# Kernel tuning notes

Measured on AMD Instinct MI355X. Metric: run time of the kernel, lower is better.

Reference implementation:

```python
import jax, jax.numpy as jnp
import numpy as np

N_NODES = 100000
N_EDGES = 1600000
NEG_SLOPE = 0.2
EPS = 1e-6


def setup_inputs() -> dict:
    key = jax.random.key(0)
    ks = jax.random.split(key, 14)
    s = 0.1  # weight init scale
    return {
        "x": jax.random.normal(ks[0], (N_NODES, 64), jnp.float32),
        "src": jax.random.randint(ks[1], (N_EDGES,), 0, N_NODES, jnp.int32),
        "dst": jax.random.randint(ks[2], (N_EDGES,), 0, N_NODES, jnp.int32),
        "W0": s * jax.random.normal(ks[3], (64, 128), jnp.float32),
        "al0": s * jax.random.normal(ks[4], (4, 32), jnp.float32),
        "ar0": s * jax.random.normal(ks[5], (4, 32), jnp.float32),
        "W1": s * jax.random.normal(ks[6], (128, 128), jnp.float32),
        "al1": s * jax.random.normal(ks[7], (4, 32), jnp.float32),
        "ar1": s * jax.random.normal(ks[8], (4, 32), jnp.float32),
        "resW1": s * jax.random.normal(ks[9], (128, 128), jnp.float32),
        "W2": s * jax.random.normal(ks[10], (128, 32), jnp.float32),
        "al2": s * jax.random.normal(ks[11], (1, 32), jnp.float32),
        "ar2": s * jax.random.normal(ks[12], (1, 32), jnp.float32),
        "resW2": s * jax.random.normal(ks[13], (128, 32), jnp.float32),
    }


def gat_conv(h, src, dst, W, al, ar, resW):
    """DGL-style GATConv. h: [N, Fin]; returns [N, H, D]."""
    H, D = al.shape
    feat = (h @ W).reshape(-1, H, D)                       # [N,H,D]
    el = jnp.sum(feat * al, axis=-1)                       # [N,H]
    er = jnp.sum(feat * ar, axis=-1)                       # [N,H]
    e = jax.nn.leaky_relu(el[src] + er[dst], NEG_SLOPE)    # [E,H]
    # segment softmax over destination nodes
    m = jax.ops.segment_max(e, dst, num_segments=N_NODES)  # [N,H]
    ex = jnp.exp(e - m[dst])                               # [E,H]
    denom = jax.ops.segment_sum(ex, dst, num_segments=N_NODES)
    alpha = ex / denom[dst]                                # [E,H]
    msg = alpha[:, :, None] * feat[src]                    # [E,H,D]
    rst = jax.ops.segment_sum(msg, dst, num_segments=N_NODES)  # [N,H,D]
    if resW is not None:
        rst = rst + (h @ resW).reshape(-1, H, D)
    return rst


def pairnorm_scs(x, scale=1.0):
    # 'PN-SCS' mode: scale-individually then center by original column mean
    col_mean = jnp.mean(x, axis=0)
    rownorm = jnp.sqrt(EPS + jnp.sum(x * x, axis=1, keepdims=True))
    return scale * x / rownorm - col_mean


def reference(x, src, dst, W0, al0, ar0, W1, al1, ar1, resW1, W2, al2, ar2, resW2):
    # layer 0: no residual, activation applied outside
    h = gat_conv(x, src, dst, W0, al0, ar0, None)          # [N,4,32]
    h = jax.nn.elu(h.reshape(h.shape[0], -1))              # [N,128]
    h = pairnorm_scs(h)
    # middle layer: residual + internal ELU (DGL applies activation inside),
    # then the outer loop flattens and applies ELU again
    h = jax.nn.elu(gat_conv(h, src, dst, W1, al1, ar1, resW1))  # [N,4,32]
    h = jax.nn.elu(h.reshape(h.shape[0], -1))              # [N,128]
    h = pairnorm_scs(h)
    # final layer: residual, mean over heads
    h = gat_conv(h, src, dst, W2, al2, ar2, resW2)         # [N,1,32]
    h = jnp.mean(h, axis=1)                                # [N,32]
    # dgl.mean_nodes readout on a single graph -> mean over nodes
    return jnp.mean(h, axis=0)                             # [32]
```

## Files before the change

kernel.cpp:

```cpp
#include <hip/hip_runtime.h>


typedef __attribute__((ext_vector_type(8))) short s8v;
typedef __attribute__((ext_vector_type(4))) float f4v;
typedef __attribute__((ext_vector_type(2))) float f2v;
typedef __attribute__((ext_vector_type(2))) _Float16 h2;
typedef __attribute__((ext_vector_type(4))) _Float16 h4;

__device__ __forceinline__ unsigned short f2bf(float f) {
  unsigned int x = __float_as_uint(f);
  x += 0x7fffu + ((x >> 16) & 1u);
  return (unsigned short)(x >> 16);
}
__device__ __forceinline__ float bf2f(unsigned short u) {
  return __uint_as_float(((unsigned int)u) << 16);
}
__device__ __forceinline__ unsigned short f2h(float f) {
  _Float16 h = (_Float16)f;
  return __builtin_bit_cast(unsigned short, h);
}
__device__ __forceinline__ unsigned char f2fp8(float v) {
  return (unsigned char)(__builtin_amdgcn_cvt_pk_fp8_f32(v, v, 0, false) & 0xff);
}
__device__ __forceinline__ float lrelu(float x) { return fmaxf(x, 0.2f * x); }
__device__ __forceinline__ float elu1(float x) { return x > 0.f ? x : __expf(x) - 1.f; }

__device__ __forceinline__ void pack_one(const float* W, const float* al, const float* ar,
                                         const float* resW, unsigned short* out,
                                         int K, int M, int BF, int H, int RES0, int t) {
  int c = t / K, k = t - c * K;
  float v = 0.f;
  if (c < BF) {
    v = W[k * BF + c];
  } else if (c < BF + H) {
    int h = c - BF;
    float s = 0.f;
    for (int d = 0; d < 32; d++) s += W[k * BF + h * 32 + d] * al[h * 32 + d];
    v = s;
  } else if (c < BF + 2 * H) {
    int h = c - BF - H;
    float s = 0.f;
    for (int d = 0; d < 32; d++) s += W[k * BF + h * 32 + d] * ar[h * 32 + d];
    v = s;
  } else if (c >= RES0) {
    v = resW[k * (M - RES0) + (c - RES0)];
  }
  unsigned short hi = f2bf(v);
  out[c * K + k] = hi;
  out[M * K + c * K + k] = f2bf(v - bf2f(hi));
}

__global__ __launch_bounds__(256) void hist_pack_k(const int* __restrict__ dst,
                                                   int* __restrict__ bhist, int E, int NB, int chunk, int P2B,
                                                   const float* __restrict__ W0, const float* __restrict__ al0,
                                                   const float* __restrict__ ar0,
                                                   const float* __restrict__ W1, const float* __restrict__ al1,
                                                   const float* __restrict__ ar1, const float* __restrict__ resW1,
                                                   const float* __restrict__ W2, const float* __restrict__ al2,
                                                   const float* __restrict__ ar2, const float* __restrict__ resW2,
                                                   unsigned short* __restrict__ w0t, unsigned short* __restrict__ w1t,
                                                   unsigned short* __restrict__ w2t) {
  if ((int)blockIdx.x < P2B) {
    __shared__ int h[512];
    for (int b = threadIdx.x; b < NB; b += 256) h[b] = 0;
    __syncthreads();
    int e0 = blockIdx.x * chunk;
    int e1 = min(E, e0 + chunk);
    for (int e = e0 + threadIdx.x; e < e1; e += 256) atomicAdd(&h[dst[e] >> 8], 1);
    __syncthreads();
    for (int b = threadIdx.x; b < NB; b += 256)
      bhist[(size_t)b * P2B + blockIdx.x] = h[b];
  } else {
    const int n0 = 144 * 64, n1 = 272 * 128, n2 = 80 * 128;
    int t = ((int)blockIdx.x - P2B) * 256 + threadIdx.x;
    if (t < n0) {
      pack_one(W0, al0, ar0, nullptr, w0t, 64, 144, 128, 4, 144, t);
    } else if (t < n0 + n1) {
      pack_one(W1, al1, ar1, resW1, w1t, 128, 272, 128, 4, 144, t - n0);
    } else if (t < n0 + n1 + n2) {
      pack_one(W2, al2, ar2, resW2, w2t, 128, 80, 32, 1, 48, t - n0 - n1);
    }
  }
}

__global__ __launch_bounds__(256) void pscan1(int* __restrict__ arr, int* __restrict__ bsum, int Nn) {
  __shared__ int s[256];
  int t = threadIdx.x;
  int base = blockIdx.x * 1024 + t * 4;
  int v0 = (base + 0 < Nn) ? arr[base + 0] : 0;
  int v1 = (base + 1 < Nn) ? arr[base + 1] : 0;
  int v2 = (base + 2 < Nn) ? arr[base + 2] : 0;
  int v3 = (base + 3 < Nn) ? arr[base + 3] : 0;
  s[t] = v0 + v1 + v2 + v3;
  __syncthreads();
  for (int off = 1; off < 256; off <<= 1) {
    int xv = (t >= off) ? s[t - off] : 0;
    __syncthreads();
    s[t] += xv;
    __syncthreads();
  }
  int excl = t ? s[t - 1] : 0;
  if (t == 255) bsum[blockIdx.x] = s[255];
  if (base + 0 < Nn) { arr[base + 0] = excl; excl += v0; }
  if (base + 1 < Nn) { arr[base + 1] = excl; excl += v1; }
  if (base + 2 < Nn) { arr[base + 2] = excl; excl += v2; }
  if (base + 3 < Nn) { arr[base + 3] = excl; }
}

__global__ __launch_bounds__(256) void pscan2(int* __restrict__ arr, const int* __restrict__ bsum,
                                              int Nn, int nb) {
  __shared__ int s[256];
  int t = threadIdx.x;
  s[t] = (t < nb) ? bsum[t] : 0;
  __syncthreads();
  for (int off = 1; off < 256; off <<= 1) {
    int xv = (t >= off) ? s[t - off] : 0;
    __syncthreads();
    s[t] += xv;
    __syncthreads();
  }
  int bb = blockIdx.x;
  int pref = bb ? s[bb - 1] : 0;
  if (pref != 0) {
    int base = bb * 1024 + t * 4;
    if (base + 0 < Nn) arr[base + 0] += pref;
    if (base + 1 < Nn) arr[base + 1] += pref;
    if (base + 2 < Nn) arr[base + 2] += pref;
    if (base + 3 < Nn) arr[base + 3] += pref;
  }
}

__global__ __launch_bounds__(256) void bscatter_k(const int* __restrict__ src, const int* __restrict__ dst,
                                                  const int* __restrict__ seg, unsigned int* __restrict__ ebuf,
                                                  int E, int NB, int chunk) {
  __shared__ int cur[512];
  for (int b = threadIdx.x; b < NB; b += 256)
    cur[b] = seg[(size_t)b * gridDim.x + blockIdx.x];
  __syncthreads();
  int e0 = blockIdx.x * chunk;
  int e1 = min(E, e0 + chunk);
  for (int e = e0 + threadIdx.x; e < e1; e += 256) {
    int d = dst[e];
    int pos = atomicAdd(&cur[d >> 8], 1);
    ebuf[pos] = ((unsigned int)src[e] << 8) | (unsigned int)(d & 255);
  }
}

__global__ __launch_bounds__(256) void fscatter_k(const unsigned int* __restrict__ ebuf,
                                                  const int* __restrict__ seg,
                                                  int* __restrict__ csr_src,
                                                  int* __restrict__ counts, int* __restrict__ rsp,
                                                  int E, int NB, int P2B, int Nn) {
  __shared__ int cnt[256];
  __shared__ int sc[256];
  __shared__ int cur[256];
  int b = blockIdx.x;
  int t = threadIdx.x;
  cnt[t] = 0;
  __syncthreads();
  int bstart = seg[(size_t)b * P2B];
  int bend = (b + 1 < NB) ? seg[(size_t)(b + 1) * P2B] : E;
  for (int e = bstart + t; e < bend; e += 256)
    atomicAdd(&cnt[ebuf[e] & 255u], 1);
  __syncthreads();
  int v = cnt[t];
  sc[t] = v;
  __syncthreads();
  for (int off = 1; off < 256; off <<= 1) {
    int xv = (t >= off) ? sc[t - off] : 0;
    __syncthreads();
    sc[t] += xv;
    __syncthreads();
  }
  int base = bstart + (t ? sc[t - 1] : 0);
  int node = (b << 8) + t;
  if (node < Nn) { counts[node] = v; rsp[node] = base; }
  cur[t] = base;
  __syncthreads();
  for (int e = bstart + t; e < bend; e += 256) {
    unsigned int sd = ebuf[e];
    int pos = atomicAdd(&cur[sd & 255u], 1);
    csr_src[pos] = (int)(sd >> 8);
  }
}

__global__ __launch_bounds__(256) void cmw_k(const float* __restrict__ colsum,
                                             const unsigned short* __restrict__ wt,
                                             float* __restrict__ cmw, int K, int M, float invN) {
  int c = blockIdx.x * 256 + threadIdx.x;
  if (c >= M) return;
  float s = 0.f;
  for (int k = 0; k < K; k++)
    s += colsum[k] * (bf2f(wt[c * K + k]) + bf2f(wt[(size_t)M * K + c * K + k]));
  cmw[c] = s * invN;
}

template <int K, int M, int R, int CG, int BF, int H, int RES0, bool AF32, bool CMW>
__global__ __launch_bounds__(256) void gemm_bf16(const void* __restrict__ Av,
                                                 const unsigned short* __restrict__ Bt,
                                                 const float* __restrict__ cmw,
                                                 unsigned char* __restrict__ feat8,
                                                 float* __restrict__ el, float* __restrict__ er,
                                                 unsigned short* __restrict__ resh, int nRowTiles) {
  int wv = (int)((blockIdx.x * blockDim.x + threadIdx.x) >> 6);
  int rowGroup = wv / CG;
  int cg = wv - rowGroup * CG;
  int tile0 = rowGroup * R;
  if (tile0 >= nRowTiles) return;
  int lane = threadIdx.x & 63;
  int r = lane & 15, q = lane >> 4;
  s8v afrag[R][K / 32];
#pragma unroll
  for (int rr = 0; rr < R; rr++) {
    if constexpr (AF32) {
      const float* arow = (const float*)Av + (size_t)((tile0 + rr) * 16 + r) * K + q * 8;
#pragma unroll
      for (int kk = 0; kk < K / 32; kk++) {
        s8v v;
#pragma unroll
        for (int j = 0; j < 8; j++) v[j] = (short)f2bf(arow[kk * 32 + j]);
        afrag[rr][kk] = v;
      }
    } else {
      const unsigned short* arow = (const unsigned short*)Av + (size_t)((tile0 + rr) * 16 + r) * K + q * 8;
#pragma unroll
      for (int kk = 0; kk < K / 32; kk++) afrag[rr][kk] = *(const s8v*)(arow + kk * 32);
    }
  }
  for (int ct = cg; ct < M / 16; ct += CG) {
    const unsigned short* brow = Bt + (size_t)(ct * 16 + r) * K + q * 8;
    s8v bhi[K / 32], blo[K / 32];
#pragma unroll
    for (int kk = 0; kk < K / 32; kk++) {
      bhi[kk] = *(const s8v*)(brow + kk * 32);
      blo[kk] = *(const s8v*)(brow + (size_t)M * K + kk * 32);
    }
    int col = ct * 16 + r;
    float cmwv = 0.f;
    if constexpr (CMW) cmwv = cmw[col];
#pragma unroll
    for (int rr = 0; rr < R; rr++) {
      f4v acc = {0.f, 0.f, 0.f, 0.f};
#pragma unroll
      for (int kk = 0; kk < K / 32; kk++) {
        acc = __builtin_amdgcn_mfma_f32_16x16x32_bf16(afrag[rr][kk], bhi[kk], acc, 0, 0, 0);
        acc = __builtin_amdgcn_mfma_f32_16x16x32_bf16(afrag[rr][kk], blo[kk], acc, 0, 0, 0);
      }
      int row0 = (tile0 + rr) * 16 + q * 4;
#pragma unroll
      for (int i = 0; i < 4; i++) {
        float v = acc[i] - cmwv;
        size_t row = (size_t)(row0 + i);
        if (col < BF) {
          feat8[row * BF + col] = f2fp8(v);
        } else if (col < BF + H) {
          el[row * H + (col - BF)] = v;
        } else if (col < BF + 2 * H) {
          er[row * H + (col - BF - H)] = v;
        } else if (RES0 < M && col >= RES0) {
          resh[row * (M - RES0) + (col - RES0)] = f2h(v);
        }
      }
    }
  }
}

template <int MODE>
__global__ __launch_bounds__(256) void aggregate4(const unsigned char* __restrict__ feat8,
                                                  const float* __restrict__ el4,
                                                  const float* __restrict__ er4,
                                                  const int* __restrict__ csr_src,
                                                  const int* __restrict__ rsp,
                                                  const int* __restrict__ counts,
                                                  const unsigned short* __restrict__ resh,
                                                  unsigned short* __restrict__ vbf,
                                                  float* __restrict__ rnrm, int Nn) {
  int n = (int)((blockIdx.x * blockDim.x + threadIdx.x) >> 6);
  if (n >= Nn) return;
  int lane = threadIdx.x & 63;
  int start = __builtin_amdgcn_readfirstlane(rsp[n]);
  int deg = __builtin_amdgcn_readfirstlane(counts[n]);
  int chunks = (deg + 15) >> 4;
  int slot = lane >> 2, h = lane & 3;
  float ern = er4[(size_t)n * 4 + h];
  int hl = lane >> 4;
  unsigned dby = (unsigned)lane << 1;
  f2v a01 = {0.f, 0.f};
  float dsum = 0.f;
  float elv = el4[(size_t)csr_src[start + slot] * 4 + h];
  for (int c = 0; c < chunks; c++) {
    const int* csp = csr_src + start + (c << 4);
    int sj[16];
#pragma unroll
    for (int j = 0; j < 16; j++) sj[j] = csp[j];
    float e = elv + ern;
    float exv = (((c << 4) + slot) < deg) ? __expf(fmaxf(e, 0.2f * e)) : 0.f;
    dsum += exv;
    if (c + 1 < chunks) elv = el4[(size_t)csp[16 + slot] * 4 + h];
#pragma unroll
    for (int j = 0; j < 16; j++) {
      float aw = __shfl(exv, (j << 2) | hl);
      unsigned short u = *(const unsigned short*)(feat8 + (((unsigned)sj[j] << 7) + dby));
      f2v fv = __builtin_amdgcn_cvt_pk_f32_fp8((int)u, false);
      f2v aw2 = {aw, aw};
      a01 = __builtin_elementwise_fma(fv, aw2, a01);
    }
  }
#pragma unroll
  for (int off = 4; off < 64; off <<= 1) dsum += __shfl_xor(dsum, off);
  float inv = dsum > 0.f ? 1.f / dsum : 0.f;
  float invh = __shfl(inv, hl);
  float v0, v1;
  if (MODE == 1) {
    h2 rr = *(const h2*)(resh + (size_t)n * 128 + lane * 2);
    v0 = elu1(elu1(a01[0] * invh + (float)rr[0]));
    v1 = elu1(elu1(a01[1] * invh + (float)rr[1]));
  } else {
    v0 = elu1(a01[0] * invh);
    v1 = elu1(a01[1] * invh);
  }
  float ss = v0 * v0 + v1 * v1;
#pragma unroll
  for (int off = 1; off < 64; off <<= 1) ss += __shfl_xor(ss, off);
  float rn = sqrtf(1e-6f + ss);
  float ri = 1.f / rn;
  unsigned int pk = (unsigned int)f2bf(v0 * ri) | ((unsigned int)f2bf(v1 * ri) << 16);
  *(unsigned int*)((char*)vbf + ((size_t)n << 8) + (lane << 2)) = pk;
  if (lane == 0) rnrm[n] = rn;
}

__global__ __launch_bounds__(256) void aggregate1(const unsigned char* __restrict__ feat8,
                                                  const float* __restrict__ el1,
                                                  const float* __restrict__ er1,
                                                  const int* __restrict__ csr_src,
                                                  const int* __restrict__ rsp,
                                                  const int* __restrict__ counts,
                                                  const unsigned short* __restrict__ res2h,
                                                  float* __restrict__ out2, int Nn) {
  int n = (int)((blockIdx.x * blockDim.x + threadIdx.x) >> 6);
  if (n >= Nn) return;
  int lane = threadIdx.x & 63;
  int start = __builtin_amdgcn_readfirstlane(rsp[n]);
  int deg = __builtin_amdgcn_readfirstlane(counts[n]);
  int chunks = (deg + 15) >> 4;
  int l16 = lane & 15;
  float ern = er1[n];
  int g = lane >> 3;
  unsigned dofs4 = (unsigned)(lane & 7) << 2;
  f2v acc01 = {0.f, 0.f}, acc23 = {0.f, 0.f};
  float dsum = 0.f;
  int sA = csr_src[start + l16];
  float elv = el1[sA];
  for (int c = 0; c < chunks; c++) {
    const int* csp = csr_src + start + (c << 4);
    float exv = (((c << 4) + l16) < deg) ? __expf(lrelu(elv + ern)) : 0.f;
    dsum += exv;
    int sAc = sA;
    if (c + 1 < chunks) {
      sA = csp[16 + l16];
      elv = el1[sA];
    }
#pragma unroll
    for (int t = 0; t < 2; t++) {
      int j = (t << 3) + g;
      int sj = __shfl(sAc, j);
      float aw = __shfl(exv, j);
      f2v aw2 = {aw, aw};
      unsigned int u = *(const unsigned int*)(feat8 + (((unsigned)sj << 5) + dofs4));
      f2v fa = __builtin_amdgcn_cvt_pk_f32_fp8((int)u, false);
      f2v fb = __builtin_amdgcn_cvt_pk_f32_fp8((int)u, true);
      acc01 = __builtin_elementwise_fma(fa, aw2, acc01);
      acc23 = __builtin_elementwise_fma(fb, aw2, acc23);
    }
  }
#pragma unroll
  for (int off = 1; off < 16; off <<= 1) dsum += __shfl_xor(dsum, off);
  float inv = dsum > 0.f ? 1.f / dsum : 0.f;
#pragma unroll
  for (int off = 8; off < 64; off <<= 1) {
    acc01[0] += __shfl_xor(acc01[0], off);
    acc01[1] += __shfl_xor(acc01[1], off);
    acc23[0] += __shfl_xor(acc23[0], off);
    acc23[1] += __shfl_xor(acc23[1], off);
  }
  if (lane < 8) {
    h4 rr = *(const h4*)(res2h + (size_t)n * 32 + (lane << 2));
    float4 o;
    o.x = acc01[0] * inv + (float)rr[0];
    o.y = acc01[1] * inv + (float)rr[1];
    o.z = acc23[0] * inv + (float)rr[2];
    o.w = acc23[1] * inv + (float)rr[3];
    *(float4*)(out2 + (size_t)n * 32 + (lane << 2)) = o;
  }
}

__global__ __launch_bounds__(256) void colsum_k(const unsigned short* __restrict__ vbf,
                                                const float* __restrict__ rnrm,
                                                float* __restrict__ colsum, int Nn) {
  __shared__ float ls[256];
  int tid = threadIdx.x;
  int c = tid & 127, rsub = tid >> 7;
  float cs = 0.f;
  for (int r = blockIdx.x * 2 + rsub; r < Nn; r += gridDim.x * 2)
    cs += bf2f(vbf[(size_t)r * 128 + c]) * rnrm[r];
  ls[tid] = cs;
  __syncthreads();
  if (tid < 128) atomicAdd(&colsum[tid], ls[tid] + ls[tid + 128]);
}

__global__ __launch_bounds__(256) void final_reduce(const float* __restrict__ out2,
                                                    float* __restrict__ outsum, int Nn) {
  __shared__ float ls[32];
  if (threadIdx.x < 32) ls[threadIdx.x] = 0.f;
  __syncthreads();
  int d = threadIdx.x & 31, rl = threadIdx.x >> 5;
  float acc = 0.f;
  for (int n = blockIdx.x * 8 + rl; n < Nn; n += gridDim.x * 8)
    acc += out2[(size_t)n * 32 + d];
  atomicAdd(&ls[d], acc);
  __syncthreads();
  if (threadIdx.x < 32) atomicAdd(&outsum[threadIdx.x], ls[threadIdx.x]);
}

__global__ void finalize_k(const float* __restrict__ outsum, float* __restrict__ out, float invN) {
  int t = threadIdx.x;
  if (t < 32) out[t] = outsum[t] * invN;
}

extern "C" void kernel_launch(void* const* d_in, const int* in_sizes, int n_in,
                              void* d_out, int out_size, void* d_ws, size_t ws_size,
                              hipStream_t stream) {
  const float* x     = (const float*)d_in[0];
  const int*   src   = (const int*)d_in[1];
  const int*   dst   = (const int*)d_in[2];
  const float* W0    = (const float*)d_in[3];
  const float* al0   = (const float*)d_in[4];
  const float* ar0   = (const float*)d_in[5];
  const float* W1    = (const float*)d_in[6];
  const float* al1   = (const float*)d_in[7];
  const float* ar1   = (const float*)d_in[8];
  const float* resW1 = (const float*)d_in[9];
  const float* W2    = (const float*)d_in[10];
  const float* al2   = (const float*)d_in[11];
  const float* ar2   = (const float*)d_in[12];
  const float* resW2 = (const float*)d_in[13];
  const int N = in_sizes[0] / 64;
  const int E = in_sizes[1];
  const float invN = 1.f / (float)N;
  const int Emax = E + 64;
  const int NB = (N + 255) >> 8;
  const int P2B = 512;
  const int chunk = (E + P2B - 1) / P2B;
  const int segN = NB * P2B;
  const int nbB = (segN + 1023) / 1024;

  char* p = (char*)d_ws;
  auto alloc = [&](size_t bytes) { char* r = p; p += (bytes + 255) & ~(size_t)255; return r; };

  char* zbase = p;
  float* colsumA = (float*)alloc(512);
  float* colsumB = (float*)alloc(512);
  float* outsum  = (float*)alloc(128);
  size_t zbytes = (size_t)(p - zbase);

  int* counts = (int*)alloc((size_t)4 * N);
  int* rsp    = (int*)alloc((size_t)4 * N);
  int* bsumB  = (int*)alloc(1024);
  int* bhist  = (int*)alloc((size_t)4 * segN);
  unsigned int* ebuf = (unsigned int*)alloc((size_t)4 * E);
  int* csr_src = (int*)alloc((size_t)4 * Emax);
  unsigned char*  feat8 = (unsigned char*)alloc((size_t)N * 128);
  unsigned short* vbf   = (unsigned short*)alloc((size_t)2 * N * 128);
  unsigned short* resh  = (unsigned short*)alloc((size_t)2 * N * 128);
  unsigned short* w0t = (unsigned short*)alloc((size_t)2 * 2 * 144 * 64);
  unsigned short* w1t = (unsigned short*)alloc((size_t)2 * 2 * 272 * 128);
  unsigned short* w2t = (unsigned short*)alloc((size_t)2 * 2 * 80 * 128);
  float* el4  = (float*)alloc((size_t)16 * N);
  float* er4  = (float*)alloc((size_t)16 * N);
  float* rnrm = (float*)alloc((size_t)4 * N);
  float* cmw1 = (float*)alloc(4 * 272);
  float* cmw2 = (float*)alloc(4 * 80);
  float* out2 = (float*)alloc((size_t)4 * N * 32);

  hipMemsetAsync(zbase, 0, zbytes, stream);
  hipMemsetAsync(csr_src + E, 0, (size_t)4 * (Emax - E), stream);

  const int packTot = 144 * 64 + 272 * 128 + 80 * 128;
  const int packBlocks = (packTot + 255) / 256;
  hist_pack_k<<<P2B + packBlocks, 256, 0, stream>>>(dst, bhist, E, NB, chunk, P2B,
                                                    W0, al0, ar0, W1, al1, ar1, resW1,
                                                    W2, al2, ar2, resW2, w0t, w1t, w2t);
  pscan1<<<nbB, 256, 0, stream>>>(bhist, bsumB, segN);
  pscan2<<<nbB, 256, 0, stream>>>(bhist, bsumB, segN, nbB);
  bscatter_k<<<P2B, 256, 0, stream>>>(src, dst, bhist, ebuf, E, NB, chunk);
  fscatter_k<<<NB, 256, 0, stream>>>(ebuf, bhist, csr_src, counts, rsp, E, NB, P2B, N);

  const int rowTiles = N / 16;
  const int rowGroups = rowTiles / 5;
  const int aggblocks = (N + 3) / 4;

  gemm_bf16<64, 144, 5, 2, 128, 4, 144, true, false><<<(rowGroups * 2 + 3) / 4, 256, 0, stream>>>(
      x, w0t, nullptr, feat8, el4, er4, nullptr, rowTiles);
  aggregate4<0><<<aggblocks, 256, 0, stream>>>(feat8, el4, er4, csr_src, rsp, counts, nullptr, vbf, rnrm, N);
  colsum_k<<<512, 256, 0, stream>>>(vbf, rnrm, colsumA, N);
  cmw_k<<<2, 256, 0, stream>>>(colsumA, w1t, cmw1, 128, 272, invN);

  gemm_bf16<128, 272, 5, 4, 128, 4, 144, false, true><<<rowGroups, 256, 0, stream>>>(
      vbf, w1t, cmw1, feat8, el4, er4, resh, rowTiles);
  aggregate4<1><<<aggblocks, 256, 0, stream>>>(feat8, el4, er4, csr_src, rsp, counts, resh, vbf, rnrm, N);
  colsum_k<<<512, 256, 0, stream>>>(vbf, rnrm, colsumB, N);
  cmw_k<<<1, 256, 0, stream>>>(colsumB, w2t, cmw2, 128, 80, invN);

  gemm_bf16<128, 80, 5, 2, 32, 1, 48, false, true><<<(rowGroups * 2 + 3) / 4, 256, 0, stream>>>(
      vbf, w2t, cmw2, feat8, el4, er4, resh, rowTiles);
  aggregate1<<<aggblocks, 256, 0, stream>>>(feat8, el4, er4, csr_src, rsp, counts, resh, out2, N);
  final_reduce<<<512, 256, 0, stream>>>(out2, outsum, N);
  finalize_k<<<1, 64, 0, stream>>>(outsum, (float*)d_out, invN);
}
```

Baseline: 552.7 us.

## Stage GEMM weight tiles in swizzled shared memory with register prefetch

The bf16 MFMA GEMM used to have each wave read its B (weight) columns straight from global memory, with waves split across column groups. Now each block of 4 waves covers 8 row tiles and walks all column tiles. Each 16-column weight tile (hi and lo bf16 planes) is loaded cooperatively into XOR-swizzled LDS, and the next tile is prefetched into registers. The goal is to cut redundant global and L2 traffic for the weights and overlap loading with compute. In exchange it adds two block barriers per column tile and uses fewer row tiles per wave (2 instead of 5), which changes A-fragment reuse and the grid shape.

```diff
diff --git a/kernel.cpp b/kernel.cpp
--- a/kernel.cpp
+++ b/kernel.cpp
@@ -195,51 +195,99 @@
   cmw[c] = s * invN;
 }
 
-template <int K, int M, int R, int CG, int BF, int H, int RES0, bool AF32, bool CMW>
+template <int K, int M, int R, int BF, int H, int RES0, bool AF32, bool CMW>
 __global__ __launch_bounds__(256) void gemm_bf16(const void* __restrict__ Av,
                                                  const unsigned short* __restrict__ Bt,
                                                  const float* __restrict__ cmw,
                                                  unsigned char* __restrict__ feat8,
                                                  float* __restrict__ el, float* __restrict__ er,
                                                  unsigned short* __restrict__ resh, int nRowTiles) {
-  int wv = (int)((blockIdx.x * blockDim.x + threadIdx.x) >> 6);
-  int rowGroup = wv / CG;
-  int cg = wv - rowGroup * CG;
-  int tile0 = rowGroup * R;
-  if (tile0 >= nRowTiles) return;
-  int lane = threadIdx.x & 63;
+  constexpr int NT = M / 16;
+  constexpr int PLANE = 16 * K * 2;
+  constexpr int RS = (K == 128) ? 8 : 7;
+  __shared__ unsigned char bbuf[2 * PLANE];
+  int t = threadIdx.x;
+  int w = t >> 6;
+  int lane = t & 63;
+  int tile0 = (int)blockIdx.x * (4 * R) + w * R;
   int r = lane & 15, q = lane >> 4;
+
   s8v afrag[R][K / 32];
+  bool valid[R];
 #pragma unroll
   for (int rr = 0; rr < R; rr++) {
-    if constexpr (AF32) {
-      const float* arow = (const float*)Av + (size_t)((tile0 + rr) * 16 + r) * K + q * 8;
-#pragma unroll
-      for (int kk = 0; kk < K / 32; kk++) {
-        s8v v;
-#pragma unroll
-        for (int j = 0; j < 8; j++) v[j] = (short)f2bf(arow[kk * 32 + j]);
-        afrag[rr][kk] = v;
+    valid[rr] = (tile0 + rr) < nRowTiles;
+    if (valid[rr]) {
+      if constexpr (AF32) {
+        const float* arow = (const float*)Av + (size_t)((tile0 + rr) * 16 + r) * K + q * 8;
+#pragma unroll
+        for (int kk = 0; kk < K / 32; kk++) {
+          s8v v;
+#pragma unroll
+          for (int j = 0; j < 8; j++) v[j] = (short)f2bf(arow[kk * 32 + j]);
+          afrag[rr][kk] = v;
+        }
+      } else {
+        const unsigned short* arow = (const unsigned short*)Av + (size_t)((tile0 + rr) * 16 + r) * K + q * 8;
+#pragma unroll
+        for (int kk = 0; kk < K / 32; kk++) afrag[rr][kk] = *(const s8v*)(arow + kk * 32);
       }
+    }
+  }
+
+  const unsigned char* gBhi = (const unsigned char*)Bt;
+  const unsigned char* gBlo = (const unsigned char*)Bt + (size_t)M * K * 2;
+
+  uint4 rh = {0, 0, 0, 0}, rl = {0, 0, 0, 0};
+  if constexpr (K == 128) {
+    rh = *(const uint4*)(gBhi + (size_t)0 * PLANE + t * 16);
+    rl = *(const uint4*)(gBlo + (size_t)0 * PLANE + t * 16);
+  } else {
+    if (t < 128) rh = *(const uint4*)(gBhi + t * 16);
+    else         rl = *(const uint4*)(gBlo + (t - 128) * 16);
+  }
+
+  for (int ct = 0; ct < NT; ct++) {
+    if constexpr (K == 128) {
+      unsigned x = (unsigned)t * 16;
+      unsigned d = x ^ (((x >> RS) & 7u) << 4);
+      *(uint4*)(bbuf + d) = rh;
+      *(uint4*)(bbuf + PLANE + d) = rl;
     } else {
-      const unsigned short* arow = (const unsigned short*)Av + (size_t)((tile0 + rr) * 16 + r) * K + q * 8;
-#pragma unroll
-      for (int kk = 0; kk < K / 32; kk++) afrag[rr][kk] = *(const s8v*)(arow + kk * 32);
-    }
-  }
-  for (int ct = cg; ct < M / 16; ct += CG) {
-    const unsigned short* brow = Bt + (size_t)(ct * 16 + r) * K + q * 8;
+      if (t < 128) {
+        unsigned x = (unsigned)t * 16;
+        unsigned d = x ^ (((x >> RS) & 7u) << 4);
+        *(uint4*)(bbuf + d) = rh;
+      } else {
+        unsigned x = (unsigned)(t - 128) * 16;
+        unsigned d = x ^ (((x >> RS) & 7u) << 4);
+        *(uint4*)(bbuf + PLANE + d) = rl;
+      }
+    }
+    __syncthreads();
+    if (ct + 1 < NT) {
+      if constexpr (K == 128) {
+        rh = *(const uint4*)(gBhi + (size_t)(ct + 1) * PLANE + t * 16);
+        rl = *(const uint4*)(gBlo + (size_t)(ct + 1) * PLANE + t * 16);
+      } else {
+        if (t < 128) rh = *(const uint4*)(gBhi + (size_t)(ct + 1) * PLANE + t * 16);
+        else         rl = *(const uint4*)(gBlo + (size_t)(ct + 1) * PLANE + (t - 128) * 16);
+      }
+    }
     s8v bhi[K / 32], blo[K / 32];
 #pragma unroll
     for (int kk = 0; kk < K / 32; kk++) {
-      bhi[kk] = *(const s8v*)(brow + kk * 32);
-      blo[kk] = *(const s8v*)(brow + (size_t)M * K + kk * 32);
+      unsigned off = (unsigned)(q * 16 + kk * 64);
+      unsigned ad = ((unsigned)r << RS) + (off ^ (((unsigned)(r & 7)) << 4));
+      bhi[kk] = *(const s8v*)(bbuf + ad);
+      blo[kk] = *(const s8v*)(bbuf + PLANE + ad);
     }
     int col = ct * 16 + r;
     float cmwv = 0.f;
     if constexpr (CMW) cmwv = cmw[col];
 #pragma unroll
     for (int rr = 0; rr < R; rr++) {
+      if (!valid[rr]) continue;
       f4v acc = {0.f, 0.f, 0.f, 0.f};
 #pragma unroll
       for (int kk = 0; kk < K / 32; kk++) {
@@ -262,6 +310,7 @@
         }
       }
     }
+    __syncthreads();
   }
 }
 
@@ -496,22 +545,22 @@
   fscatter_k<<<NB, 256, 0, stream>>>(ebuf, bhist, csr_src, counts, rsp, E, NB, P2B, N);
 
   const int rowTiles = N / 16;
-  const int rowGroups = rowTiles / 5;
+  const int gblocks = (rowTiles + 7) / 8;
   const int aggblocks = (N + 3) / 4;
 
-  gemm_bf16<64, 144, 5, 2, 128, 4, 144, true, false><<<(rowGroups * 2 + 3) / 4, 256, 0, stream>>>(
+  gemm_bf16<64, 144, 2, 128, 4, 144, true, false><<<gblocks, 256, 0, stream>>>(
       x, w0t, nullptr, feat8, el4, er4, nullptr, rowTiles);
   aggregate4<0><<<aggblocks, 256, 0, stream>>>(feat8, el4, er4, csr_src, rsp, counts, nullptr, vbf, rnrm, N);
   colsum_k<<<512, 256, 0, stream>>>(vbf, rnrm, colsumA, N);
   cmw_k<<<2, 256, 0, stream>>>(colsumA, w1t, cmw1, 128, 272, invN);
 
-  gemm_bf16<128, 272, 5, 4, 128, 4, 144, false, true><<<rowGroups, 256, 0, stream>>>(
+  gemm_bf16<128, 272, 2, 128, 4, 144, false, true><<<gblocks, 256, 0, stream>>>(
       vbf, w1t, cmw1, feat8, el4, er4, resh, rowTiles);
   aggregate4<1><<<aggblocks, 256, 0, stream>>>(feat8, el4, er4, csr_src, rsp, counts, resh, vbf, rnrm, N);
   colsum_k<<<512, 256, 0, stream>>>(vbf, rnrm, colsumB, N);
   cmw_k<<<1, 256, 0, stream>>>(colsumB, w2t, cmw2, 128, 80, invN);
 
-  gemm_bf16<128, 80, 5, 2, 32, 1, 48, false, true><<<(rowGroups * 2 + 3) / 4, 256, 0, stream>>>(
+  gemm_bf16<128, 80, 2, 32, 1, 48, false, true><<<gblocks, 256, 0, stream>>>(
       vbf, w2t, cmw2, feat8, el4, er4, resh, rowTiles);
   aggregate1<<<aggblocks, 256, 0, stream>>>(feat8, el4, er4, csr_src, rsp, counts, resh, out2, N);
   final_reduce<<<512, 256, 0, stream>>>(out2, outsum, N);
```

Result: faster. 488.8 us (-11.6%).
